# Optimization experiments

Measured on AMD Instinct MI355X. Metric: run time of the kernel, lower is better.

The kernel has to match this reference:

```python
import jax, jax.numpy as jnp
import numpy as np

B, L, D = 256, 256, 128          # batch, max_len, embedding_dim
H = W = 16                       # H=int(sqrt(L)), W=L//H
N, CBD = 128, 1024               # embedding_num, code_book_dim = N*8 = D*8
BETA = 0.25
BN_EPS = 1e-3                    # tf.layers.batch_normalization default


def _conv(x, w, b):
    return jax.lax.conv_general_dilated(x, w, (1, 1), 'VALID',
        dimension_numbers=('NHWC', 'HWIO', 'NHWC')) + b


def _convT(x, w, b):
    return jax.lax.conv_transpose(x, w, (1, 1), 'VALID',
        dimension_numbers=('NHWC', 'HWIO', 'NHWC')) + b


def _bn(x, g, b):
    # inference-mode BN with moving_mean=0, moving_var=1 (tf.layers default training=False)
    return g * (x * (1.0 / np.sqrt(1.0 + BN_EPS))) + b


def setup_inputs() -> dict:
    key = jax.random.key(0)
    ks = jax.random.split(key, 24)
    rn = lambda k, s, sc=0.05: (jax.random.normal(k, s, dtype=jnp.float32) * sc)
    inp = {
        'x': jax.random.normal(ks[0], (B, L, D), dtype=jnp.float32),
        'mask': jnp.ones((B, L), dtype=jnp.float32),
        'code_book': jax.random.normal(ks[1], (N, CBD), dtype=jnp.float32),
        # encoder: conv2d k=2 valid, channels D -> 2D -> 4D -> 8D
        'ew1': rn(ks[2], (2, 2, D, 2 * D)), 'eb1': jnp.zeros((2 * D,), jnp.float32),
        'eg1': jnp.ones((2 * D,), jnp.float32), 'ebt1': jnp.zeros((2 * D,), jnp.float32),
        'ew2': rn(ks[3], (2, 2, 2 * D, 4 * D)), 'eb2': jnp.zeros((4 * D,), jnp.float32),
        'eg2': jnp.ones((4 * D,), jnp.float32), 'ebt2': jnp.zeros((4 * D,), jnp.float32),
        'ew3': rn(ks[4], (2, 2, 4 * D, 8 * D)), 'eb3': jnp.zeros((8 * D,), jnp.float32),
        # decoder: conv2d_transpose k=2 valid, channels 8D -> 4D -> 2D -> D
        'dw1': rn(ks[5], (2, 2, 8 * D, 4 * D)), 'db1': jnp.zeros((4 * D,), jnp.float32),
        'dg1': jnp.ones((4 * D,), jnp.float32), 'dbt1': jnp.zeros((4 * D,), jnp.float32),
        'dw2': rn(ks[6], (2, 2, 4 * D, 2 * D)), 'db2': jnp.zeros((2 * D,), jnp.float32),
        'dg2': jnp.ones((2 * D,), jnp.float32), 'dbt2': jnp.zeros((2 * D,), jnp.float32),
        'dw3': rn(ks[7], (2, 2, 2 * D, D)), 'db3': jnp.zeros((D,), jnp.float32),
    }
    return inp


def reference(x, mask, code_book,
              ew1, eb1, eg1, ebt1, ew2, eb2, eg2, ebt2, ew3, eb3,
              dw1, db1, dg1, dbt1, dw2, db2, dg2, dbt2, dw3, db3):
    # ---- encoder (conv branch) ----
    xi = x.reshape(-1, H, W, D)                                   # [B,16,16,D]
    h = jax.nn.relu(_bn(_conv(xi, ew1, eb1), eg1, ebt1))          # [B,15,15,2D]
    h = jax.nn.relu(_bn(_conv(h, ew2, eb2), eg2, ebt2))           # [B,14,14,4D]
    x_encode = _conv(h, ew3, eb3)                                 # [B,13,13,8D]

    # ---- VQ codebook lookup (get_quantized) ----
    flat = x_encode.reshape(-1, CBD)                              # [B*169, CBD]
    dist = (jnp.sum(flat ** 2, axis=1, keepdims=True)
            + jnp.sum(code_book ** 2, axis=1)
            - 2.0 * flat @ code_book.T)                           # [B*169, N]
    idx = jnp.argmin(dist, axis=1)
    quantized = code_book[idx].reshape(x_encode.shape)            # gather == one_hot @ code_book

    # ---- straight-through + decoder ----
    ste = x_encode + jax.lax.stop_gradient(quantized - x_encode)
    h = jax.nn.relu(_bn(_convT(ste, dw1, db1), dg1, dbt1))        # [B,14,14,4D]
    h = jax.nn.relu(_bn(_convT(h, dw2, db2), dg2, dbt2))          # [B,15,15,2D]
    vq = _convT(h, dw3, db3)                                      # [B,16,16,D]
    vq_x = vq.reshape(-1, L, D)

    vq_mean = jnp.sum(vq_x, axis=1) / jnp.sum(mask, axis=-1, keepdims=True)

    recon = jnp.mean((x - vq_x) ** 2)
    vq_l = jnp.mean((quantized - jax.lax.stop_gradient(x_encode)) ** 2)
    commit = jnp.mean((x_encode - jax.lax.stop_gradient(quantized)) ** 2)
    vqvae_loss = recon + vq_l + BETA * commit
    return (vq_mean, vq_x, x_encode, quantized, vqvae_loss)
```

## Files before the change

kernel.cpp:

```cpp
#include <hip/hip_runtime.h>
#include <math.h>

typedef float f4 __attribute__((ext_vector_type(4)));
typedef short s8 __attribute__((ext_vector_type(8)));

#define WS_FLOATS 66000000L
__device__ float g_fallback[WS_FLOATS];

__device__ __forceinline__ f4 ldg4(const float* p) { return *(const f4*)p; }

__device__ __forceinline__ unsigned short bfr(float x) {
    unsigned int u = __float_as_uint(x);
    u += 0x7fffu + ((u >> 16) & 1u);
    return (unsigned short)(u >> 16);
}
__device__ __forceinline__ float bff(unsigned short h) {
    return __uint_as_float(((unsigned int)h) << 16);
}
__device__ __forceinline__ s8 z8() { s8 z = {0,0,0,0,0,0,0,0}; return z; }

__device__ __forceinline__ void split8(const f4& x0, const f4& x1, s8& hi, s8& lo) {
#pragma unroll
    for (int e = 0; e < 4; ++e) {
        unsigned short h0 = bfr(x0[e]);
        hi[e] = (short)h0; lo[e] = (short)bfr(x0[e] - bff(h0));
        unsigned short h1 = bfr(x1[e]);
        hi[e + 4] = (short)h1; lo[e + 4] = (short)bfr(x1[e] - bff(h1));
    }
}

template<int SPLIT, int ASRC, int EPI, int OUTF>
__global__ __launch_bounds__(256, 2)
void mfma_conv(const void* __restrict__ aHi, const void* __restrict__ aLo,
               const short* __restrict__ wHi, const short* __restrict__ wLo,
               const float* __restrict__ bias, const float* __restrict__ gamma,
               const float* __restrict__ beta,
               void* __restrict__ oHi, void* __restrict__ oLo,
               int* __restrict__ idxo,
               const float* __restrict__ xref, float* __restrict__ colsum,
               double* __restrict__ sacc,
               int IH, int IW, int Cin, int cinShift, int OHOW, int OW,
               int N, int K, int off, int ntShift, float bns)
{
    constexpr int PL = 128 * 64;
    constexpr int NPL = (SPLIT == 1) ? 3 : 4;
    __shared__ short smem[NPL * PL];
    short* Ah = smem;
    short* Al  = smem + PL;
    short* BhS = smem + 2 * PL;
    short* BlS = smem + 3 * PL;

    const int tid = threadIdx.x;
    const int lane = tid & 63, wid = tid >> 6;
    const int fr = lane & 15, fq = lane >> 4;
    const int wm = (wid >> 1) * 64, wn = (wid & 1) * 64;

    int m0, n0;
    {
        const int nwg = gridDim.x;
        const int bid = blockIdx.x;
        const int q = nwg >> 3, r = nwg & 7;
        const int xcd = bid & 7, c = bid >> 3;
        const int wg = (xcd < r ? xcd * (q + 1) : r * (q + 1) + (xcd - r) * q) + c;
        const int NTm1 = (1 << ntShift) - 1;
        m0 = (wg >> ntShift) * 128;
        n0 = (wg & NTm1) * 128;
    }

    const int sr = tid >> 1;
    const int skh = (tid & 1) << 5;

    long tapOff[4]; bool tv[4];
    {
        int m = m0 + sr;
        int b = m / OHOW; int rem = m - b * OHOW;
        int oi = rem / OW; int oj = rem - oi * OW;
#pragma unroll
        for (int t = 0; t < 4; ++t) {
            int ii = oi + (t >> 1) + off, jj = oj + (t & 1) + off;
            bool v = (ii >= 0) && (ii < IH) && (jj >= 0) && (jj < IW);
            tv[t] = v;
            tapOff[t] = ((long)b * IH + (v ? ii : 0)) * IW + (v ? jj : 0);
        }
    }

    f4 acc[4][4];
#pragma unroll
    for (int a = 0; a < 4; ++a)
#pragma unroll
        for (int b = 0; b < 4; ++b) acc[a][b] = (f4){0.f, 0.f, 0.f, 0.f};

    const short* wHrow = wHi + (long)(n0 + sr) * K;
    const short* wLrow = (SPLIT == 2) ? (wLo + (long)(n0 + sr) * K) : nullptr;

    const int swzW = (sr & 7) << 3;
    const int sbase = sr * 64;

    s8 rah[4], ral[4], rbh[4], rbl[4];
    f4 rax0[4], rax1[4];

    auto LOADREGS = [&](int kc) {
        const int kk = kc + skh;
        const int t = kk >> cinShift;
        const int ci = kk & (Cin - 1);
        const bool v = tv[t];
        if (ASRC == 0) {
            const float* p = (const float*)aHi + tapOff[t] * Cin + ci;
#pragma unroll
            for (int q = 0; q < 4; ++q) {
                rax0[q] = v ? ldg4(p + 8 * q) : (f4){0.f,0.f,0.f,0.f};
                rax1[q] = v ? ldg4(p + 8 * q + 4) : (f4){0.f,0.f,0.f,0.f};
            }
        } else if (ASRC == 1) {
            const short* ph = (const short*)aHi + tapOff[t] * Cin + ci;
            const short* pl = (const short*)aLo + tapOff[t] * Cin + ci;
#pragma unroll
            for (int q = 0; q < 4; ++q) {
                rah[q] = v ? *(const s8*)(ph + 8 * q) : z8();
                ral[q] = v ? *(const s8*)(pl + 8 * q) : z8();
            }
        } else {
            const short* ph = (const short*)aHi + tapOff[t] * Cin + ci;
#pragma unroll
            for (int q = 0; q < 4; ++q) rah[q] = v ? *(const s8*)(ph + 8 * q) : z8();
        }
        if (SPLIT == 2) {
#pragma unroll
            for (int q = 0; q < 4; ++q) {
                rbh[q] = *(const s8*)(wHrow + kc + skh + 8 * q);
                rbl[q] = *(const s8*)(wLrow + kc + skh + 8 * q);
            }
        }
    };

    auto STORE = [&]() {
        if (ASRC == 0) {
#pragma unroll
            for (int q = 0; q < 4; ++q) split8(rax0[q], rax1[q], rah[q], ral[q]);
        }
#pragma unroll
        for (int q = 0; q < 4; ++q) {
            int kx = (skh + 8 * q) ^ swzW;
            *(s8*)&Ah[sbase + kx] = rah[q];
            if (SPLIT == 2) {
                *(s8*)&Al[sbase + kx]  = ral[q];
                *(s8*)&BhS[sbase + kx] = rbh[q];
                *(s8*)&BlS[sbase + kx] = rbl[q];
            }
        }
    };

    auto stageB = [&](int bsel, int kc2) {
        short* bb = smem + (1 + bsel) * PL;
        const int rr0 = wid << 5;
#pragma unroll
        for (int i = 0; i < 4; ++i) {
            const int r = rr0 + 8 * i + (lane >> 3);
            const int c = lane & 7;
            const short* src = wHi + (long)(n0 + r) * K + kc2 + 8 * (c ^ (r & 7));
            __builtin_amdgcn_global_load_lds(
                (const __attribute__((address_space(1))) void*)src,
                (__attribute__((address_space(3))) void*)(bb + (rr0 + 8 * i) * 64),
                16, 0, 0);
        }
    };

    int bcur = 0;
    LOADREGS(0);
    if (SPLIT == 1) stageB(0, 0);

    for (int kc = 0; kc < K; kc += 64) {
        if (SPLIT == 1) {
            asm volatile("s_waitcnt lgkmcnt(0)" ::: "memory");
            __builtin_amdgcn_s_barrier();
            STORE();
            if (kc + 64 < K) {
                stageB(bcur ^ 1, kc + 64);
                asm volatile("s_waitcnt vmcnt(4)" ::: "memory");
            } else {
                asm volatile("s_waitcnt vmcnt(0)" ::: "memory");
            }
            __builtin_amdgcn_sched_barrier(0);
            asm volatile("s_waitcnt lgkmcnt(0)" ::: "memory");
            __builtin_amdgcn_s_barrier();
        } else {
            __syncthreads();
            STORE();
            __syncthreads();
        }
        if (kc + 64 < K) LOADREGS(kc + 64);

        const short* Bc = (SPLIT == 1) ? (smem + (1 + bcur) * PL) : BhS;

        __builtin_amdgcn_s_setprio(1);
#pragma unroll
        for (int ks = 0; ks < 2; ++ks) {
            const int colk = ks * 32 + fq * 8;
            s8 afh[4], afl[4], bfh[4], bfl[4];
#pragma unroll
            for (int mf = 0; mf < 4; ++mf) {
                int ar = wm + mf * 16 + fr;
                int ai = ar * 64 + (colk ^ ((ar & 7) << 3));
                afh[mf] = *(const s8*)&Ah[ai];
                if (SPLIT == 2) afl[mf] = *(const s8*)&Al[ai];
            }
#pragma unroll
            for (int nf = 0; nf < 4; ++nf) {
                int br = wn + nf * 16 + fr;
                int bi2 = br * 64 + (colk ^ ((br & 7) << 3));
                bfh[nf] = *(const s8*)&Bc[bi2];
                if (SPLIT == 2) bfl[nf] = *(const s8*)&BlS[bi2];
            }
#pragma unroll
            for (int mf = 0; mf < 4; ++mf)
#pragma unroll
                for (int nf = 0; nf < 4; ++nf) {
                    acc[mf][nf] = __builtin_amdgcn_mfma_f32_16x16x32_bf16(
                        afh[mf], bfh[nf], acc[mf][nf], 0, 0, 0);
                    if (SPLIT == 2) {
                        acc[mf][nf] = __builtin_amdgcn_mfma_f32_16x16x32_bf16(
                            afh[mf], bfl[nf], acc[mf][nf], 0, 0, 0);
                        acc[mf][nf] = __builtin_amdgcn_mfma_f32_16x16x32_bf16(
                            afl[mf], bfh[nf], acc[mf][nf], 0, 0, 0);
                    }
                }
        }
        __builtin_amdgcn_s_setprio(0);
        bcur ^= 1;
    }

    if (EPI == 2) {
        __syncthreads();
        float* pbv = (float*)smem;
        int*   piv = (int*)((float*)smem + 256);
        float cnv[4];
#pragma unroll
        for (int nf = 0; nf < 4; ++nf) cnv[nf] = bias[n0 + wn + nf * 16 + fr];
#pragma unroll
        for (int mf = 0; mf < 4; ++mf)
#pragma unroll
            for (int j = 0; j < 4; ++j) {
                float best = 3.4e38f; int bi = 0;
#pragma unroll
                for (int nf = 0; nf < 4; ++nf) {
                    float d = cnv[nf] - 2.0f * acc[mf][nf][j];
                    int col = wn + nf * 16 + fr;
                    if (d < best) { best = d; bi = col; }
                }
#pragma unroll
                for (int sh = 1; sh <= 8; sh <<= 1) {
                    float ov = __shfl_xor(best, sh, 64);
                    int ob = __shfl_xor(bi, sh, 64);
                    if (ov < best || (ov == best && ob < bi)) { best = ov; bi = ob; }
                }
                if (fr == 0) {
                    int r = wm + mf * 16 + fq * 4 + j;
                    pbv[(wid & 1) * 128 + r] = best;
                    piv[(wid & 1) * 128 + r] = bi;
                }
            }
        __syncthreads();
        double win = 0.0;
        if (tid < 128) {
            float b0 = pbv[tid], b1 = pbv[128 + tid];
            int i0 = piv[tid], i1 = piv[128 + tid];
            idxo[m0 + tid] = (b1 < b0) ? i1 : i0;
            win = (double)((b1 < b0) ? b1 : b0);
        }
        __syncthreads();
        double* rd = (double*)smem;
        rd[tid] = win; __syncthreads();
        for (int h = 128; h; h >>= 1) {
            if (tid < h) rd[tid] += rd[tid + h];
            __syncthreads();
        }
        if (tid == 0) atomicAdd(sacc, rd[0]);
        return;
    }

    float bi[4], ga[4], be[4];
#pragma unroll
    for (int nf = 0; nf < 4; ++nf) {
        int col = n0 + wn + nf * 16 + fr;
        bi[nf] = bias[col];
        if (EPI == 1) { ga[nf] = gamma[col]; be[nf] = beta[col]; }
    }
    double tsum = 0.0;
    float csum[4] = {0.f, 0.f, 0.f, 0.f};
#pragma unroll
    for (int mf = 0; mf < 4; ++mf)
#pragma unroll
        for (int j = 0; j < 4; ++j) {
            long gm = m0 + wm + mf * 16 + fq * 4 + j;
#pragma unroll
            for (int nf = 0; nf < 4; ++nf) {
                int col = n0 + wn + nf * 16 + fr;
                float vv = acc[mf][nf][j] + bi[nf];
                if (EPI == 1) {
                    vv = ga[nf] * (vv * bns) + be[nf];
                    vv = fmaxf(vv, 0.f);
                }
                long o = gm * (long)N + col;
                if (OUTF == 0) {
                    ((float*)oHi)[o] = vv;
                } else if (OUTF == 2) {
                    ((short*)oHi)[o] = (short)bfr(vv);
                } else {
                    unsigned short h = bfr(vv);
                    ((short*)oHi)[o] = (short)h;
                    ((short*)oLo)[o] = (short)bfr(vv - bff(h));
                }
                if (EPI == 3) tsum += (double)vv * vv;
                if (EPI == 4) {
                    float d = vv - xref[o];
                    tsum += (double)d * d;
                    csum[nf] += vv;
                }
            }
        }
    if (EPI == 4) {
        int bb128 = (m0 >> 8) * 128;
#pragma unroll
        for (int nf = 0; nf < 4; ++nf)
            atomicAdd(&colsum[bb128 + n0 + wn + nf * 16 + fr], csum[nf]);
    }
    if (EPI == 3 || EPI == 4) {
        __syncthreads();
        double* rd = (double*)smem;
        rd[tid] = tsum; __syncthreads();
        for (int h = 128; h; h >>= 1) {
            if (tid < h) rd[tid] += rd[tid + h];
            __syncthreads();
        }
        if (tid == 0) atomicAdd(sacc, rd[0]);
    }
}

__global__ void prep_all(const float* __restrict__ ew1, const float* __restrict__ ew2,
                         const float* __restrict__ ew3, const float* __restrict__ dw1,
                         const float* __restrict__ dw2, const float* __restrict__ dw3,
                         const float* __restrict__ cb,
                         short* __restrict__ ewt1h, short* __restrict__ ewt1l,
                         short* __restrict__ ewt2h, short* __restrict__ ewt2l,
                         short* __restrict__ ewt3h,
                         short* __restrict__ dwt1Th, short* __restrict__ dwt1Tl,
                         short* __restrict__ dwt2h, short* __restrict__ dwt3h,
                         short* __restrict__ cbh, short* __restrict__ cbl,
                         float* __restrict__ zbuf)
{
    int b = blockIdx.x;
    int t = threadIdx.x;
    if (b < 512) {
        int i = b * 256 + t; int n = i >> 9, k = i & 511;
        float x = ew1[(long)k * 256 + n]; unsigned short h = bfr(x);
        ewt1h[i] = (short)h; ewt1l[i] = (short)bfr(x - bff(h));
    } else if (b < 2560) {
        int i = (b - 512) * 256 + t; int n = i >> 10, k = i & 1023;
        float x = ew2[(long)k * 512 + n]; unsigned short h = bfr(x);
        ewt2h[i] = (short)h; ewt2l[i] = (short)bfr(x - bff(h));
    } else if (b < 10752) {
        int i = (b - 2560) * 256 + t; int n = i >> 11, k = i & 2047;
        ewt3h[i] = (short)bfr(ew3[(long)k * 1024 + n]);
    } else if (b < 18944) {
        int i = (b - 10752) * 256 + t; int Np = i >> 10, co = i & 1023;
        int tt = Np >> 9, nn = Np & 511;
        float x = dw1[((long)(tt * 1024 + co)) * 512 + nn]; unsigned short h = bfr(x);
        dwt1Th[i] = (short)h; dwt1Tl[i] = (short)bfr(x - bff(h));
    } else if (b < 20992) {
        int i = (b - 18944) * 256 + t; int n = i >> 11, k = i & 2047;
        dwt2h[i] = (short)bfr(dw2[(long)k * 256 + n]);
    } else if (b < 21504) {
        int i = (b - 20992) * 256 + t; int n = i >> 10, k = i & 1023;
        dwt3h[i] = (short)bfr(dw3[(long)k * 128 + n]);
    } else if (b < 22016) {
        int i = (b - 21504) * 256 + t;
        float x = cb[i]; unsigned short h = bfr(x);
        cbh[i] = (short)h; cbl[i] = (short)bfr(x - bff(h));
    } else {
        int i = (b - 22016) * 256 + t; if (i < 2048) zbuf[i] = 0.f;
    }
}

__global__ void wsplitT(const float* __restrict__ p1, short* __restrict__ hi,
                        short* __restrict__ lo)
{
    int i = blockIdx.x * 256 + threadIdx.x;
    if (i >= 262144) return;
    int n = i >> 11, k = i & 2047;
    float x = p1[(long)k * 128 + n];
    unsigned short h = bfr(x);
    hi[i] = (short)h;
    lo[i] = (short)bfr(x - bff(h));
}

__global__ void code_bias(const float* __restrict__ cb, const float* __restrict__ eb3,
                          float* __restrict__ bias2)
{
    int c = blockIdx.x * 4 + (threadIdx.x >> 6);
    int lane = threadIdx.x & 63;
    if (c >= 128) return;
    const f4* p = (const f4*)(cb + (long)c * 1024);
    const f4* e = (const f4*)eb3;
    float s2 = 0.f, su = 0.f;
#pragma unroll
    for (int q = 0; q < 4; ++q) {
        f4 v = p[q * 64 + lane];
        f4 w = e[q * 64 + lane];
        s2 += (v[0]*v[0] + v[1]*v[1]) + (v[2]*v[2] + v[3]*v[3]);
        su += (v[0]*w[0] + v[1]*w[1]) + (v[2]*w[2] + v[3]*w[3]);
    }
#pragma unroll
    for (int sh = 32; sh; sh >>= 1) {
        s2 += __shfl_xor(s2, sh, 64);
        su += __shfl_xor(su, sh, 64);
    }
    if (lane == 0) bias2[c] = s2 - 2.f * su;
}

__global__ __launch_bounds__(256)
void d1_gather(const float* __restrict__ CD, const int* __restrict__ idx,
               const float* __restrict__ db1, const float* __restrict__ dg1,
               const float* __restrict__ dbt1, short* __restrict__ out, float bns)
{
    int m = blockIdx.x * 4 + (threadIdx.x >> 6);
    int lane = threadIdx.x & 63;
    if (m >= 50176) return;
    int b = m / 196, rem = m - b * 196;
    int oi = rem / 14, oj = rem - oi * 14;
    float2 acc[4];
#pragma unroll
    for (int q = 0; q < 4; ++q) acc[q] = make_float2(0.f, 0.f);
#pragma unroll
    for (int t = 0; t < 4; ++t) {
        int ii = oi - 1 + (t >> 1), jj = oj - 1 + (t & 1);
        if (ii >= 0 && ii < 13 && jj >= 0 && jj < 13) {
            int c = idx[(b * 13 + ii) * 13 + jj];
            const float2* p = (const float2*)(CD + ((long)c * 2048 + t * 512));
#pragma unroll
            for (int q = 0; q < 4; ++q) {
                float2 v = p[lane + 64 * q];
                acc[q].x += v.x; acc[q].y += v.y;
            }
        }
    }
#pragma unroll
    for (int q = 0; q < 4; ++q) {
        int n = 2 * (lane + 64 * q);
        float v0 = fmaxf(dg1[n]     * ((acc[q].x + db1[n])     * bns) + dbt1[n],     0.f);
        float v1 = fmaxf(dg1[n + 1] * ((acc[q].y + db1[n + 1]) * bns) + dbt1[n + 1], 0.f);
        short2 s2v;
        s2v.x = (short)bfr(v0); s2v.y = (short)bfr(v1);
        ((short2*)out)[(long)m * 256 + lane + 64 * q] = s2v;
    }
}

__global__ void gather_rows(const float* __restrict__ cb, const int* __restrict__ idx,
                            float* __restrict__ q)
{
    int m = blockIdx.x;
    int c = idx[m];
    const f4* src = (const f4*)(cb + (long)c * 1024);
    f4* dst = (f4*)(q + (long)m * 1024);
    dst[threadIdx.x] = src[threadIdx.x];
}

__global__ void finalize2(const double* __restrict__ s, float* __restrict__ loss)
{
    if (threadIdx.x == 0)
        loss[0] = (float)(s[0] / 8388608.0 + 1.25 * ((s[1] + s[2]) / 44302336.0));
}

__global__ void vq_mean_fin(const float* __restrict__ colsum,
                            const float* __restrict__ mask, float* __restrict__ o)
{
    __shared__ float red[128];
    int b = blockIdx.x;
    int d = threadIdx.x;
    red[d] = mask[b * 256 + d] + mask[b * 256 + 128 + d];
    __syncthreads();
    for (int h = 64; h; h >>= 1) { if (d < h) red[d] += red[d + h]; __syncthreads(); }
    o[b * 128 + d] = colsum[b * 128 + d] / red[0];
}

extern "C" void kernel_launch(void* const* d_in, const int* in_sizes, int n_in,
                              void* d_out, int out_size, void* d_ws, size_t ws_size,
                              hipStream_t stream)
{
    const float* x    = (const float*)d_in[0];
    const float* mask = (const float*)d_in[1];
    const float* cb   = (const float*)d_in[2];
    const float* ew1 = (const float*)d_in[3];
    const float* eb1 = (const float*)d_in[4];
    const float* eg1 = (const float*)d_in[5];
    const float* ebt1= (const float*)d_in[6];
    const float* ew2 = (const float*)d_in[7];
    const float* eb2 = (const float*)d_in[8];
    const float* eg2 = (const float*)d_in[9];
    const float* ebt2= (const float*)d_in[10];
    const float* ew3 = (const float*)d_in[11];
    const float* eb3 = (const float*)d_in[12];
    const float* dw1 = (const float*)d_in[13];
    const float* db1 = (const float*)d_in[14];
    const float* dg1 = (const float*)d_in[15];
    const float* dbt1= (const float*)d_in[16];
    const float* dw2 = (const float*)d_in[17];
    const float* db2 = (const float*)d_in[18];
    const float* dg2 = (const float*)d_in[19];
    const float* dbt2= (const float*)d_in[20];
    const float* dw3 = (const float*)d_in[21];
    const float* db3 = (const float*)d_in[22];

    float* out = (float*)d_out;
    float* o_vqmean = out;
    float* o_vqx    = out + 32768;
    float* o_xe     = out + 8421376;
    float* o_q      = out + 52723712;
    float* o_loss   = out + 97026048;

    float* base;
    if (ws_size >= (size_t)WS_FLOATS * 4) {
        base = (float*)d_ws;
    } else {
        void* p = nullptr;
        hipGetSymbolAddress(&p, HIP_SYMBOL(g_fallback));
        base = (float*)p;
    }

    float* cur = base;
    short* h1h = (short*)cur; cur += 7372800;
    short* h1l = (short*)cur; cur += 7372800;
    short* h2h = (short*)cur; cur += 12845056;
    short* h2l = (short*)cur; cur += 12845056;
    short* d1o = (short*)cur; cur += 12845056;
    short* d2o = (short*)cur; cur += 7372800;
    short* ewt1h = (short*)cur; cur += 65536;
    short* ewt1l = (short*)cur; cur += 65536;
    short* ewt2h = (short*)cur; cur += 262144;
    short* ewt2l = (short*)cur; cur += 262144;
    short* ewt3h = (short*)cur; cur += 1048576;
    short* dwt1Th = (short*)cur; cur += 1048576;
    short* dwt1Tl = (short*)cur; cur += 1048576;
    short* dwt2h = (short*)cur; cur += 262144;
    short* dwt3h = (short*)cur; cur += 65536;
    short* cbh   = (short*)cur; cur += 65536;
    short* cbl   = (short*)cur; cur += 65536;
    float* P1raw = cur; cur += 262144;
    short* wvh   = (short*)cur; cur += 131072;
    short* wvl   = (short*)cur; cur += 131072;
    float* CDt   = cur; cur += 262144;
    float* bias2 = cur; cur += 128;
    float* zbuf  = cur; cur += 2048;
    int* idxb = (int*)cur; cur += 43264;
    float* colsum = cur; cur += 32768;
    double* sdbl = (double*)cur; cur += 16;

    const float bns = (float)(1.0 / sqrt(1.0 + 1e-3));

    hipMemsetAsync(colsum, 0, 32768 * sizeof(float), stream);
    hipMemsetAsync(sdbl, 0, 3 * sizeof(double), stream);
    prep_all<<<22024, 256, 0, stream>>>(ew1, ew2, ew3, dw1, dw2, dw3, cb,
        ewt1h, ewt1l, ewt2h, ewt2l, ewt3h, dwt1Th, dwt1Tl, dwt2h, dwt3h,
        cbh, cbl, zbuf);
    code_bias<<<32, 256, 0, stream>>>(cb, eb3, bias2);

    mfma_conv<2, 0, 0, 0><<<16, 256, 0, stream>>>(
        ew3, nullptr, cbh, cbl, zbuf, nullptr, nullptr, P1raw, nullptr, nullptr,
        nullptr, nullptr, nullptr,
        2, 2050, 1024, 10, 2048, 2048, 128, 1024, 0, 0, bns);
    wsplitT<<<1024, 256, 0, stream>>>(P1raw, wvh, wvl);
    mfma_conv<2, 0, 0, 0><<<16, 256, 0, stream>>>(
        cb, nullptr, dwt1Th, dwt1Tl, zbuf, nullptr, nullptr, CDt, nullptr, nullptr,
        nullptr, nullptr, nullptr,
        2, 130, 1024, 10, 128, 128, 2048, 1024, 0, 4, bns);

    mfma_conv<2, 0, 1, 1><<<900, 256, 0, stream>>>(
        x, nullptr, ewt1h, ewt1l, eb1, eg1, ebt1, h1h, h1l, nullptr,
        nullptr, nullptr, nullptr,
        16, 16, 128, 7, 225, 15, 256, 512, 0, 1, bns);
    mfma_conv<2, 1, 1, 1><<<1568, 256, 0, stream>>>(
        h1h, h1l, ewt2h, ewt2l, eb2, eg2, ebt2, h2h, h2l, nullptr,
        nullptr, nullptr, nullptr,
        15, 15, 256, 8, 196, 14, 512, 1024, 0, 2, bns);
    mfma_conv<1, 2, 3, 0><<<2704, 256, 0, stream>>>(
        h2h, nullptr, ewt3h, nullptr, eb3, nullptr, nullptr, o_xe, nullptr, nullptr,
        nullptr, nullptr, sdbl + 1,
        14, 14, 512, 9, 169, 13, 1024, 2048, 0, 3, bns);

    mfma_conv<2, 1, 2, 0><<<338, 256, 0, stream>>>(
        h2h, h2l, wvh, wvl, bias2, nullptr, nullptr, nullptr, nullptr, idxb,
        nullptr, nullptr, sdbl + 2,
        14, 14, 512, 9, 169, 13, 128, 2048, 0, 0, bns);
    gather_rows<<<43264, 256, 0, stream>>>(cb, idxb, o_q);

    d1_gather<<<12544, 256, 0, stream>>>(CDt, idxb, db1, dg1, dbt1, d1o, bns);
    mfma_conv<1, 2, 1, 2><<<900, 256, 0, stream>>>(
        d1o, nullptr, dwt2h, nullptr, db2, dg2, dbt2, d2o, nullptr, nullptr,
        nullptr, nullptr, nullptr,
        14, 14, 512, 9, 225, 15, 256, 2048, -1, 1, bns);
    mfma_conv<1, 2, 4, 0><<<512, 256, 0, stream>>>(
        d2o, nullptr, dwt3h, nullptr, db3, nullptr, nullptr, o_vqx, nullptr, nullptr,
        x, colsum, sdbl + 0,
        15, 15, 256, 8, 256, 16, 128, 1024, -1, 0, bns);

    vq_mean_fin<<<256, 128, 0, stream>>>(colsum, mask, o_vqmean);
    finalize2<<<1, 64, 0, stream>>>(sdbl, o_loss);
}
```

Measured before the change: 912.3 us.

## Add 256x256-tile bf16 MFMA implicit-GEMM kernel for two conv stages

```diff
diff --git a/kernel.cpp b/kernel.cpp
--- a/kernel.cpp
+++ b/kernel.cpp
@@ -26,6 +26,194 @@
         hi[e] = (short)h0; lo[e] = (short)bfr(x0[e] - bff(h0));
         unsigned short h1 = bfr(x1[e]);
         hi[e + 4] = (short)h1; lo[e + 4] = (short)bfr(x1[e] - bff(h1));
+    }
+}
+
+template<int EPI>
+__global__ __launch_bounds__(512, 2)
+void gemm256(const short* __restrict__ aSrc, const short* __restrict__ wHi,
+             const float* __restrict__ bias, const float* __restrict__ gamma,
+             const float* __restrict__ beta, void* __restrict__ oHi,
+             double* __restrict__ sacc, const short* __restrict__ zsrc,
+             int IH, int IW, int OHOW, int OW, int N, int K, int off,
+             int ntShift, float bns)
+{
+    extern __shared__ short smem[];
+
+    const int tid = threadIdx.x;
+    const int w = tid >> 6;
+    const int l = tid & 63;
+    const int lr = l >> 3;
+    const int lc = l & 7;
+    const int fr = l & 15, fq = l >> 4;
+    const int wm = (w >> 2) * 128;
+    const int wn = (w & 3) * 64;
+
+    int m0, n0;
+    {
+        const int nwg = gridDim.x;
+        const int bid = blockIdx.x;
+        const int q = nwg >> 3, r = nwg & 7;
+        const int xcd = bid & 7, c = bid >> 3;
+        const int wg = (xcd < r ? xcd * (q + 1) : r * (q + 1) + (xcd - r) * q) + c;
+        const int NTm1 = (1 << ntShift) - 1;
+        m0 = (wg >> ntShift) * 256;
+        n0 = (wg & NTm1) * 256;
+    }
+
+    int bOff[4], oiA[4], ojA[4], bRowB[4];
+#pragma unroll
+    for (int i = 0; i < 4; ++i) {
+        int row = (w << 5) + (i << 3) + lr;
+        int m = m0 + row;
+        int b = m / OHOW; int rem = m - b * OHOW;
+        oiA[i] = rem / OW; ojA[i] = rem - oiA[i] * OW;
+        bOff[i] = b * IH * IW;
+        bRowB[i] = (n0 + row) * K;
+    }
+    const int swz = (lc ^ lr) << 3;
+
+    auto stage = [&](int sel, int kc) {
+        short* Ab = smem + sel * 16384;
+        short* Bb = smem + 32768 + sel * 16384;
+        const int t = kc >> 9;
+        const int ci = (kc & 511) + swz;
+        const int di = (t >> 1) + off, dj = (t & 1) + off;
+#pragma unroll
+        for (int i = 0; i < 4; ++i) {
+            int ii = oiA[i] + di, jj = ojA[i] + dj;
+            bool v = (ii >= 0) && (ii < IH) && (jj >= 0) && (jj < IW);
+            const short* sA = v ? aSrc + (long)(bOff[i] + ii * IW + jj) * 512 + ci
+                                : zsrc + (l << 3);
+            __builtin_amdgcn_global_load_lds(
+                (const __attribute__((address_space(1))) void*)sA,
+                (__attribute__((address_space(3))) void*)(Ab + (((w << 5) + (i << 3)) * 64)),
+                16, 0, 0);
+            const short* sB = wHi + bRowB[i] + kc + swz;
+            __builtin_amdgcn_global_load_lds(
+                (const __attribute__((address_space(1))) void*)sB,
+                (__attribute__((address_space(3))) void*)(Bb + (((w << 5) + (i << 3)) * 64)),
+                16, 0, 0);
+        }
+    };
+
+    f4 acc[8][4];
+#pragma unroll
+    for (int a = 0; a < 8; ++a)
+#pragma unroll
+        for (int b = 0; b < 4; ++b) acc[a][b] = (f4){0.f, 0.f, 0.f, 0.f};
+
+    const int NT = K >> 6;
+    stage(0, 0);
+    stage(1, 64);
+
+    for (int t = 0; t < NT; ++t) {
+        const int sel = t & 1;
+        const short* Ab = smem + sel * 16384;
+        const short* Bb = smem + 32768 + sel * 16384;
+
+        if (t < NT - 1) asm volatile("s_waitcnt vmcnt(8)" ::: "memory");
+        else            asm volatile("s_waitcnt vmcnt(0)" ::: "memory");
+        __builtin_amdgcn_s_barrier();
+        __builtin_amdgcn_sched_barrier(0);
+
+        s8 af[8], bf[4];
+#pragma unroll
+        for (int mf = 0; mf < 8; ++mf) {
+            int row = wm + mf * 16 + fr;
+            int c = fq ^ (row & 7);
+            af[mf] = *(const s8*)&Ab[row * 64 + (c << 3)];
+        }
+#pragma unroll
+        for (int nf = 0; nf < 4; ++nf) {
+            int row = wn + nf * 16 + fr;
+            int c = fq ^ (row & 7);
+            bf[nf] = *(const s8*)&Bb[row * 64 + (c << 3)];
+        }
+        asm volatile("s_waitcnt lgkmcnt(0)" ::: "memory");
+        __builtin_amdgcn_sched_barrier(0);
+        __builtin_amdgcn_s_setprio(1);
+#pragma unroll
+        for (int mf = 0; mf < 8; ++mf)
+#pragma unroll
+            for (int nf = 0; nf < 4; ++nf)
+                acc[mf][nf] = __builtin_amdgcn_mfma_f32_16x16x32_bf16(
+                    af[mf], bf[nf], acc[mf][nf], 0, 0, 0);
+        __builtin_amdgcn_s_setprio(0);
+
+#pragma unroll
+        for (int mf = 0; mf < 8; ++mf) {
+            int row = wm + mf * 16 + fr;
+            int c = (4 + fq) ^ (row & 7);
+            af[mf] = *(const s8*)&Ab[row * 64 + (c << 3)];
+        }
+#pragma unroll
+        for (int nf = 0; nf < 4; ++nf) {
+            int row = wn + nf * 16 + fr;
+            int c = (4 + fq) ^ (row & 7);
+            bf[nf] = *(const s8*)&Bb[row * 64 + (c << 3)];
+        }
+        asm volatile("s_waitcnt lgkmcnt(0)" ::: "memory");
+        __builtin_amdgcn_sched_barrier(0);
+        __builtin_amdgcn_s_barrier();
+        __builtin_amdgcn_sched_barrier(0);
+        if (t + 2 < NT) stage(sel, (t + 2) << 6);
+
+        __builtin_amdgcn_s_setprio(1);
+#pragma unroll
+        for (int mf = 0; mf < 8; ++mf)
+#pragma unroll
+            for (int nf = 0; nf < 4; ++nf)
+                acc[mf][nf] = __builtin_amdgcn_mfma_f32_16x16x32_bf16(
+                    af[mf], bf[nf], acc[mf][nf], 0, 0, 0);
+        __builtin_amdgcn_s_setprio(0);
+    }
+
+    if (EPI == 3) {
+        float bi[4];
+#pragma unroll
+        for (int nf = 0; nf < 4; ++nf) bi[nf] = bias[n0 + wn + nf * 16 + fr];
+        double tsum = 0.0;
+#pragma unroll
+        for (int mf = 0; mf < 8; ++mf)
+#pragma unroll
+            for (int j = 0; j < 4; ++j) {
+                long gm = m0 + wm + mf * 16 + fq * 4 + j;
+                float* orow = (float*)oHi + gm * (long)N + n0;
+#pragma unroll
+                for (int nf = 0; nf < 4; ++nf) {
+                    float v = acc[mf][nf][j] + bi[nf];
+                    orow[wn + nf * 16 + fr] = v;
+                    tsum += (double)v * v;
+                }
+            }
+        __syncthreads();
+        double* rd = (double*)smem;
+        rd[tid] = tsum; __syncthreads();
+        for (int h = 256; h; h >>= 1) {
+            if (tid < h) rd[tid] += rd[tid + h];
+            __syncthreads();
+        }
+        if (tid == 0) atomicAdd(sacc, rd[0]);
+    } else {
+        float bi[4], ga[4], be[4];
+#pragma unroll
+        for (int nf = 0; nf < 4; ++nf) {
+            int col = n0 + wn + nf * 16 + fr;
+            bi[nf] = bias[col]; ga[nf] = gamma[col]; be[nf] = beta[col];
+        }
+#pragma unroll
+        for (int mf = 0; mf < 8; ++mf)
+#pragma unroll
+            for (int j = 0; j < 4; ++j) {
+                long gm = m0 + wm + mf * 16 + fq * 4 + j;
+                short* orow = (short*)oHi + gm * (long)N + n0;
+#pragma unroll
+                for (int nf = 0; nf < 4; ++nf) {
+                    float v = ga[nf] * ((acc[mf][nf][j] + bi[nf]) * bns) + be[nf];
+                    orow[wn + nf * 16 + fr] = (short)bfr(fmaxf(v, 0.f));
+                }
+            }
     }
 }
 
@@ -556,6 +744,11 @@
 
     const float bns = (float)(1.0 / sqrt(1.0 + 1e-3));
 
+    hipFuncSetAttribute(reinterpret_cast<const void*>(&gemm256<3>),
+                        hipFuncAttributeMaxDynamicSharedMemorySize, 131072);
+    hipFuncSetAttribute(reinterpret_cast<const void*>(&gemm256<1>),
+                        hipFuncAttributeMaxDynamicSharedMemorySize, 131072);
+
     hipMemsetAsync(colsum, 0, 32768 * sizeof(float), stream);
     hipMemsetAsync(sdbl, 0, 3 * sizeof(double), stream);
     prep_all<<<22024, 256, 0, stream>>>(ew1, ew2, ew3, dw1, dw2, dw3, cb,
@@ -581,10 +774,9 @@
         h1h, h1l, ewt2h, ewt2l, eb2, eg2, ebt2, h2h, h2l, nullptr,
         nullptr, nullptr, nullptr,
         15, 15, 256, 8, 196, 14, 512, 1024, 0, 2, bns);
-    mfma_conv<1, 2, 3, 0><<<2704, 256, 0, stream>>>(
-        h2h, nullptr, ewt3h, nullptr, eb3, nullptr, nullptr, o_xe, nullptr, nullptr,
-        nullptr, nullptr, sdbl + 1,
-        14, 14, 512, 9, 169, 13, 1024, 2048, 0, 3, bns);
+    gemm256<3><<<676, 512, 131072, stream>>>(
+        h2h, ewt3h, eb3, nullptr, nullptr, o_xe, sdbl + 1, (const short*)zbuf,
+        14, 14, 169, 13, 1024, 2048, 0, 2, bns);
 
     mfma_conv<2, 1, 2, 0><<<338, 256, 0, stream>>>(
         h2h, h2l, wvh, wvl, bias2, nullptr, nullptr, nullptr, nullptr, idxb,
@@ -593,10 +785,9 @@
     gather_rows<<<43264, 256, 0, stream>>>(cb, idxb, o_q);
 
     d1_gather<<<12544, 256, 0, stream>>>(CDt, idxb, db1, dg1, dbt1, d1o, bns);
-    mfma_conv<1, 2, 1, 2><<<900, 256, 0, stream>>>(
-        d1o, nullptr, dwt2h, nullptr, db2, dg2, dbt2, d2o, nullptr, nullptr,
-        nullptr, nullptr, nullptr,
-        14, 14, 512, 9, 225, 15, 256, 2048, -1, 1, bns);
+    gemm256<1><<<225, 512, 131072, stream>>>(
+        d1o, dwt2h, db2, dg2, dbt2, d2o, nullptr, (const short*)zbuf,
+        14, 14, 225, 15, 256, 2048, -1, 0, bns);
     mfma_conv<1, 2, 4, 0><<<512, 256, 0, stream>>>(
         d2o, nullptr, dwt3h, nullptr, db3, nullptr, nullptr, o_vqx, nullptr, nullptr,
         x, colsum, sdbl + 0,
```

Measured after the change: 901.4 us. Within noise of the previous version (-1.2%).
